# Optimization experiments

Hardware: AMD Instinct MI355X
Metric: run time of the kernel (lower is better)

Reference implementation:

```python
import jax, jax.numpy as jnp
import numpy as np

N = 50000      # cells (nodes)
E = 800000     # kNN edges
IN = 50        # PCA dims
HID = 64       # hidden_dim
HEADS = 4
C = HID // HEADS  # per-head channels = 16
L = 3          # num_layers
NC = 12        # num_classes
INV_SQRT_C = 1.0 / np.sqrt(C)
LN_EPS = 1e-5


def setup_inputs() -> dict:
    key = jax.random.key(0)
    ks = iter(jax.random.split(key, 32))
    def w(shape, fan_in):
        return jax.random.normal(next(ks), shape, jnp.float32) / np.sqrt(fan_in)
    inp = {
        'x': jax.random.normal(next(ks), (N, IN), jnp.float32),
        'edge_index': jax.random.randint(next(ks), (2, E), 0, N, jnp.int32),
        'edge_attr': jax.random.uniform(next(ks), (E,), jnp.float32),
        # input projection
        'Win': w((IN, HID), IN), 'b_in': jnp.zeros((HID,), jnp.float32),
        # per-layer TransformerConv params (stacked over L)
        'Wq': w((L, HID, HID), HID), 'bq': jnp.zeros((L, HID), jnp.float32),
        'Wk': w((L, HID, HID), HID), 'bk': jnp.zeros((L, HID), jnp.float32),
        'Wv': w((L, HID, HID), HID), 'bv': jnp.zeros((L, HID), jnp.float32),
        'Wedge': w((L, 1, HID), 1),                      # lin_edge, bias=False
        'Wskip': w((L, HID, HID), HID), 'bskip': jnp.zeros((L, HID), jnp.float32),
        'Wbeta': w((L, 3 * HID, 1), 3 * HID),            # lin_beta, bias=False
        'ln_g': jnp.ones((L, HID), jnp.float32), 'ln_b': jnp.zeros((L, HID), jnp.float32),
        # classifier MLP
        'Wc1': w((HID, HID), HID), 'bc1': jnp.zeros((HID,), jnp.float32),
        'Wc2': w((HID, NC), HID), 'bc2': jnp.zeros((NC,), jnp.float32),
    }
    return inp


def _layer_norm(z, g, b):
    mu = z.mean(-1, keepdims=True)
    var = ((z - mu) ** 2).mean(-1, keepdims=True)
    return (z - mu) / jnp.sqrt(var + LN_EPS) * g + b


def reference(x, edge_index, edge_attr, Win, b_in, Wq, bq, Wk, bk, Wv, bv,
              Wedge, Wskip, bskip, Wbeta, ln_g, ln_b, Wc1, bc1, Wc2, bc2):
    n = x.shape[0]
    src, dst = edge_index[0], edge_index[1]   # messages flow src -> dst
    ea = edge_attr[:, None]                    # (E,1)
    h = x @ Win + b_in                         # (N,HID)
    for i in range(L):
        h_res = h
        q = (h @ Wq[i] + bq[i]).reshape(n, HEADS, C)
        k = (h @ Wk[i] + bk[i]).reshape(n, HEADS, C)
        v = (h @ Wv[i] + bv[i]).reshape(n, HEADS, C)
        e = (ea @ Wedge[i]).reshape(-1, HEADS, C)        # (E,H,C)
        kj = k[src] + e                                   # edge-gathered keys + edge feat
        alpha = jnp.einsum('ehc,ehc->eh', q[dst], kj) * INV_SQRT_C  # (E,H)
        # segment softmax over destination nodes
        amax = jax.ops.segment_max(alpha, dst, num_segments=n)
        amax = jnp.where(jnp.isfinite(amax), amax, 0.0)
        ex = jnp.exp(alpha - amax[dst])
        denom = jax.ops.segment_sum(ex, dst, num_segments=n)
        p = ex / (denom[dst] + 1e-16)
        msg = (v[src] + e) * p[..., None]                 # (E,H,C)
        out = jax.ops.segment_sum(msg, dst, num_segments=n).reshape(n, HID)
        # beta-gated skip
        x_r = h @ Wskip[i] + bskip[i]
        beta = jax.nn.sigmoid(jnp.concatenate([out, x_r, out - x_r], -1) @ Wbeta[i])  # (N,1)
        out = beta * x_r + (1.0 - beta) * out
        h = _layer_norm(out + h_res, ln_g[i], ln_b[i])
    h1 = jax.nn.relu(h @ Wc1 + bc1)
    return h1 @ Wc2 + bc2
```

## Files before the change

### kernel.cpp

```cpp
#include <hip/hip_runtime.h>
#include <hip/hip_fp16.h>
#include <math.h>

#define IN_F 50
#define HID 64
#define NC 12
#define LN_EPS 1e-5f

#define BSH 8
#define BSZ 256
#define CHUNK 8192
#define PCAP 8192

typedef _Float16 half8 __attribute__((ext_vector_type(8)));
typedef _Float16 half4_t __attribute__((ext_vector_type(4)));
typedef float float4v __attribute__((ext_vector_type(4)));


__global__ void count_kernel(const int* __restrict__ dst, int* __restrict__ cnt, int e) {
  int i = blockIdx.x * blockDim.x + threadIdx.x;
  if (i < e) atomicAdd(&cnt[dst[i]], 1);
}

__global__ __launch_bounds__(256) void scan_reduce_kernel(const int* __restrict__ cnt,
                                                          int* __restrict__ part, int n) {
  int base = blockIdx.x * 1024;
  int sum = 0;
  for (int i = threadIdx.x; i < 1024; i += 256) {
    int g = base + i;
    if (g < n) sum += cnt[g];
  }
#pragma unroll
  for (int off = 1; off < 64; off <<= 1) sum += __shfl_xor(sum, off);
  __shared__ int ws[4];
  if ((threadIdx.x & 63) == 0) ws[threadIdx.x >> 6] = sum;
  __syncthreads();
  if (threadIdx.x == 0) part[blockIdx.x] = ws[0] + ws[1] + ws[2] + ws[3];
}

__global__ void scan_part_kernel(int* __restrict__ part, int nb, int* __restrict__ total) {
  int lane = threadIdx.x;
  int orig = (lane < nb) ? part[lane] : 0;
  int v = orig;
#pragma unroll
  for (int off = 1; off < 64; off <<= 1) {
    int t = __shfl_up(v, off);
    if (lane >= off) v += t;
  }
  if (lane < nb) part[lane] = v - orig;
  if (lane == 63) *total = v;
}

__global__ __launch_bounds__(256) void scan_apply_kernel(const int* __restrict__ cnt,
    const int* __restrict__ part, int* __restrict__ rowptr, int n) {
  int base = blockIdx.x * 1024;
  int t = threadIdx.x;
  int vals[4];
  int lsum = 0;
#pragma unroll
  for (int j = 0; j < 4; j++) {
    int g = base + t * 4 + j;
    vals[j] = (g < n) ? cnt[g] : 0;
    lsum += vals[j];
  }
  int v = lsum;
#pragma unroll
  for (int off = 1; off < 64; off <<= 1) {
    int tv = __shfl_up(v, off);
    if ((t & 63) >= off) v += tv;
  }
  __shared__ int wsum[4];
  if ((t & 63) == 63) wsum[t >> 6] = v;
  __syncthreads();
  int wbase = 0;
  int w = t >> 6;
#pragma unroll
  for (int j = 0; j < 4; j++) if (j < w) wbase += wsum[j];
  int excl = v - lsum + wbase + part[blockIdx.x];
#pragma unroll
  for (int j = 0; j < 4; j++) {
    int g = base + t * 4 + j;
    if (g < n) rowptr[g] = excl;
    excl += vals[j];
  }
}

__global__ void cursor_init_kernel(const int* __restrict__ rowptr,
                                   int* __restrict__ cursor, int n, int nbk) {
  int b = blockIdx.x * blockDim.x + threadIdx.x;
  if (b < nbk) cursor[b] = rowptr[min(b * BSZ, n)];
}

__global__ __launch_bounds__(256) void bucket_kernel(
    const int* __restrict__ src, const int* __restrict__ dst,
    const float* __restrict__ ea, int* __restrict__ cursor,
    unsigned long long* __restrict__ rec_stage,
    unsigned short* __restrict__ dloc_stage, int e)
{
  __shared__ int bcnt[256];
  __shared__ int gbase[256];
  __shared__ int bfill[256];
  int tid = threadIdx.x;
  bcnt[tid] = 0; bfill[tid] = 0;
  __syncthreads();
  int cb = blockIdx.x * CHUNK;
  int ce = min(cb + CHUNK, e);
  for (int i = cb + tid; i < ce; i += 256)
    atomicAdd(&bcnt[dst[i] >> BSH], 1);
  __syncthreads();
  if (bcnt[tid] > 0) gbase[tid] = atomicAdd(&cursor[tid], bcnt[tid]);
  __syncthreads();
  for (int i = cb + tid; i < ce; i += 256) {
    int d = dst[i];
    int b = d >> BSH;
    int slot = atomicAdd(&bfill[b], 1);
    int pos = gbase[b] + slot;
    rec_stage[pos] =
        ((unsigned long long)__float_as_uint(ea[i]) << 32) | (unsigned int)src[i];
    dloc_stage[pos] = (unsigned short)(d & (BSZ - 1));
  }
}

__global__ __launch_bounds__(256) void place_kernel(
    const int* __restrict__ rowptr,
    const unsigned long long* __restrict__ rec_stage,
    const unsigned short* __restrict__ dloc_stage,
    unsigned long long* __restrict__ edges, int n)
{
  extern __shared__ char smem[];
  unsigned long long* sbuf = (unsigned long long*)smem;
  int* lrp  = (int*)(smem + (size_t)PCAP * 8);
  int* lcnt = lrp + BSZ;
  int lo = blockIdx.x * BSZ;
  int hi = min(lo + BSZ, n);
  int nb = hi - lo;
  int tid = threadIdx.x;
  if (tid < nb) { lrp[tid] = rowptr[lo + tid]; lcnt[tid] = 0; }
  __syncthreads();
  int base = rowptr[lo];
  int cnt  = rowptr[hi] - base;
  for (int i = tid; i < cnt; i += 256) {
    unsigned long long rec = rec_stage[base + i];
    int dl = dloc_stage[base + i];
    int slot = (lrp[dl] - base) + atomicAdd(&lcnt[dl], 1);
    if (slot < PCAP) sbuf[slot] = rec;
    else edges[(size_t)base + slot] = rec;
  }
  __syncthreads();
  int lim = min(cnt, PCAP);
  for (int i = tid; i < lim; i += 256)
    edges[(size_t)base + i] = sbuf[i];
}


__global__ __launch_bounds__(256) void wprep_kernel(
    const float* __restrict__ Wq, const float* __restrict__ Wk,
    const float* __restrict__ Wv, const float* __restrict__ Ws,
    const float* __restrict__ Wc1, const float* __restrict__ Win,
    const float* __restrict__ bq, const float* __restrict__ bk,
    const float* __restrict__ bv, const float* __restrict__ bs,
    const float* __restrict__ bc1, const float* __restrict__ bin,
    _Float16* __restrict__ Wt, float* __restrict__ biasP)
{
  int idx = blockIdx.x * 256 + threadIdx.x;
  if (idx >= 896 * 64) return;
  int col = idx >> 6, k = idx & 63;
  float w, b;
  if (col < 768) {
    int l = col >> 8, rem = col & 255;
    int mat = rem >> 6, c = rem & 63;
    const float* W  = (mat == 0) ? Wq : (mat == 1) ? Wk : (mat == 2) ? Wv : Ws;
    const float* bb = (mat == 0) ? bq : (mat == 1) ? bk : (mat == 2) ? bv : bs;
    w = W[((size_t)l * 64 + k) * 64 + c];
    b = bb[l * 64 + c];
  } else if (col < 832) {
    int c = col - 768;
    w = Wc1[k * 64 + c];
    b = bc1[c];
  } else {
    int c = col - 832;
    w = (k < IN_F) ? Win[k * 64 + c] : 0.f;
    b = bin[c];
  }
  Wt[idx] = (_Float16)w;
  if (k == 0) biasP[col] = b;
}


template<int NMAT, int MODE, bool RELU>
__global__ __launch_bounds__(256) void gemm_mfma(
    const float* __restrict__ A, int lda, int kin, int M,
    const _Float16* __restrict__ Wt, const float* __restrict__ biasP,
    float* __restrict__ C, int ldc,
    float* __restrict__ qx, __half* __restrict__ kvb)
{
  __shared__ __align__(16) _Float16 hsh[64 * 72];
  constexpr int KVSZ = (MODE == 1) ? 64 * 128 : 8;
  __shared__ __align__(16) __half kvsh[KVSZ];

  const int tid = threadIdx.x;
  const int wave = tid >> 6, lane = tid & 63;
  const int lrow = lane & 15, quad = lane >> 4;
  const int row0 = blockIdx.x * 64;
  constexpr int WPC = 4 / NMAT;
  const int cg = wave / WPC;
  const int wi = wave % WPC;

  half8 bf[4][2];
  const _Float16* wbase = Wt + (size_t)cg * 64 * 64;
#pragma unroll
  for (int ct = 0; ct < 4; ct++)
#pragma unroll
    for (int ks = 0; ks < 2; ks++)
      bf[ct][ks] = *(const half8*)&wbase[(ct * 16 + lrow) * 64 + ks * 32 + quad * 8];
  float bv_[4];
#pragma unroll
  for (int ct = 0; ct < 4; ct++) bv_[ct] = biasP[cg * 64 + ct * 16 + lrow];

  if (kin == 64) {
    int r = tid >> 2, cq = tid & 3;
    int grow = row0 + r;
#pragma unroll
    for (int i = 0; i < 4; i++) {
      int c0 = cq * 16 + i * 4;
      float4 v = make_float4(0.f, 0.f, 0.f, 0.f);
      if (grow < M) v = *(const float4*)&A[(size_t)grow * lda + c0];
      half4_t hv;
      hv[0] = (_Float16)v.x; hv[1] = (_Float16)v.y;
      hv[2] = (_Float16)v.z; hv[3] = (_Float16)v.w;
      *(half4_t*)&hsh[r * 72 + c0] = hv;
    }
  } else {
    for (int idx = tid; idx < 64 * 64; idx += 256) {
      int r = idx >> 6, c = idx & 63;
      int grow = row0 + r;
      float v = (grow < M && c < kin) ? A[(size_t)grow * lda + c] : 0.f;
      hsh[r * 72 + c] = (_Float16)v;
    }
  }
  __syncthreads();

  float4v acc[NMAT][4];
#pragma unroll
  for (int rt = 0; rt < NMAT; rt++)
#pragma unroll
    for (int ct = 0; ct < 4; ct++) {
      acc[rt][ct][0] = bv_[ct]; acc[rt][ct][1] = bv_[ct];
      acc[rt][ct][2] = bv_[ct]; acc[rt][ct][3] = bv_[ct];
    }

#pragma unroll
  for (int rt = 0; rt < NMAT; rt++) {
    int rbase = (wi * NMAT + rt) * 16;
#pragma unroll
    for (int ks = 0; ks < 2; ks++) {
      half8 af = *(const half8*)&hsh[(rbase + lrow) * 72 + ks * 32 + quad * 8];
#pragma unroll
      for (int ct = 0; ct < 4; ct++)
        acc[rt][ct] = __builtin_amdgcn_mfma_f32_16x16x32_f16(af, bf[ct][ks],
                                                             acc[rt][ct], 0, 0, 0);
    }
  }

  if (MODE == 0) {
#pragma unroll
    for (int rt = 0; rt < NMAT; rt++) {
      int rbase = (wi * NMAT + rt) * 16;
#pragma unroll
      for (int reg = 0; reg < 4; reg++) {
        int row = row0 + rbase + quad * 4 + reg;
        if (row < M) {
#pragma unroll
          for (int ct = 0; ct < 4; ct++) {
            float v = acc[rt][ct][reg];
            if (RELU) v = fmaxf(v, 0.f);
            C[(size_t)row * ldc + cg * 64 + ct * 16 + lrow] = v;
          }
        }
      }
    }
  } else {
    if (cg == 0 || cg == 3) {
      int cofs = (cg == 0) ? 0 : 64;
#pragma unroll
      for (int rt = 0; rt < 4; rt++) {
#pragma unroll
        for (int reg = 0; reg < 4; reg++) {
          int row = row0 + rt * 16 + quad * 4 + reg;
          if (row < M) {
#pragma unroll
            for (int ct = 0; ct < 4; ct++)
              qx[(size_t)row * 128 + cofs + ct * 16 + lrow] = acc[rt][ct][reg];
          }
        }
      }
    } else {
      int cofs = (cg == 1) ? 0 : 64;
#pragma unroll
      for (int rt = 0; rt < 4; rt++)
#pragma unroll
        for (int reg = 0; reg < 4; reg++) {
          int rloc = rt * 16 + quad * 4 + reg;
#pragma unroll
          for (int ct = 0; ct < 4; ct++)
            kvsh[rloc * 128 + cofs + ct * 16 + lrow] = __float2half(acc[rt][ct][reg]);
        }
    }
    __syncthreads();
    for (int idx = tid; idx < 1024; idx += 256) {
      int r = idx >> 4, c4 = idx & 15;
      int grow = row0 + r;
      if (grow < M) {
        uint2 kk = *(const uint2*)&kvsh[r * 128 + c4 * 4];
        uint2 vv = *(const uint2*)&kvsh[r * 128 + 64 + c4 * 4];
        uint4 o; o.x = kk.x; o.y = kk.y; o.z = vv.x; o.w = vv.y;
        *(uint4*)&kvb[(size_t)grow * 128 + c4 * 8] = o;
      }
    }
  }
}


__global__ __launch_bounds__(256) void attn_post_kernel(
    const int* __restrict__ rowptr, const unsigned long long* __restrict__ edges,
    const float* __restrict__ qx, const uint4* __restrict__ kvb,
    const float* __restrict__ wedge, const float* __restrict__ wbeta,
    const float* __restrict__ lng, const float* __restrict__ lnb,
    float* __restrict__ h, int n)
{
  int lane = threadIdx.x & 63;
  int node = blockIdx.x * 4 + (threadIdx.x >> 6);
  if (node >= n) return;
  int grp = lane >> 4;
  int c4 = lane & 15;
  const float4* row4 = (const float4*)qx;
  float4 q4 = row4[(size_t)node * 32 + c4];
  float4 we4 = ((const float4*)wedge)[c4];
  const float SC = 0.25f * 1.44269504f;
  float4 qs;
  qs.x = q4.x * SC; qs.y = q4.y * SC; qs.z = q4.z * SC; qs.w = q4.w * SC;
  float qwe = qs.x * we4.x + qs.y * we4.y + qs.z * we4.z + qs.w * we4.w;
  int s0 = rowptr[node], s1 = rowptr[node + 1];
  float l = 0.f, pa = 0.f;
  float ax = 0.f, ay = 0.f, az = 0.f, aw = 0.f;
  for (int cb = s0; cb < s1; cb += 64) {
    int cnt = min(64, s1 - cb);
    unsigned long long rec64 = (lane < cnt) ? edges[cb + lane] : 0ull;
    unsigned int my_src = (unsigned int)(rec64 & 0xffffffffu);
    unsigned int my_ea  = (unsigned int)(rec64 >> 32);
    for (int j = 0; j * 4 < cnt; j++) {
      int sl = j * 4 + grp;
      bool valid = sl < cnt;
      int srcn   = (int)__shfl(my_src, sl);
      float a    = __uint_as_float(__shfl(my_ea, sl));
      uint4 kv = kvb[(size_t)srcn * 16 + c4];
      float2 k01 = __half22float2(*(__half2*)&kv.x);
      float2 k23 = __half22float2(*(__half2*)&kv.y);
      float2 v01 = __half22float2(*(__half2*)&kv.z);
      float2 v23 = __half22float2(*(__half2*)&kv.w);
      float prod = qs.x * k01.x + qs.y * k01.y + qs.z * k23.x + qs.w * k23.y
                 + a * qwe;
      prod += __shfl_xor(prod, 1);
      prod += __shfl_xor(prod, 2);
      float p = valid ? exp2f(prod) : 0.f;
      l  += p;
      pa += p * a;
      ax += p * v01.x;
      ay += p * v01.y;
      az += p * v23.x;
      aw += p * v23.y;
    }
  }
  ax += pa * we4.x; ay += pa * we4.y; az += pa * we4.z; aw += pa * we4.w;
  ax += __shfl_xor(ax, 16); ax += __shfl_xor(ax, 32);
  ay += __shfl_xor(ay, 16); ay += __shfl_xor(ay, 32);
  az += __shfl_xor(az, 16); az += __shfl_xor(az, 32);
  aw += __shfl_xor(aw, 16); aw += __shfl_xor(aw, 32);
  l  += __shfl_xor(l, 16);  l  += __shfl_xor(l, 32);
  float inv = 1.f / (l + 1e-16f);
  float ox = ax * inv, oy = ay * inv, oz = az * inv, ow = aw * inv;
  float4 xr = row4[(size_t)node * 32 + 16 + c4];
  float4 hr = ((const float4*)h)[(size_t)node * 16 + c4];
  float4 w1 = ((const float4*)wbeta)[c4];
  float4 w2 = ((const float4*)wbeta)[16 + c4];
  float4 w3 = ((const float4*)wbeta)[32 + c4];
  float sv = ox * w1.x + oy * w1.y + oz * w1.z + ow * w1.w
           + xr.x * w2.x + xr.y * w2.y + xr.z * w2.z + xr.w * w2.w
           + (ox - xr.x) * w3.x + (oy - xr.y) * w3.y
           + (oz - xr.z) * w3.z + (ow - xr.w) * w3.w;
  sv += __shfl_xor(sv, 1); sv += __shfl_xor(sv, 2);
  sv += __shfl_xor(sv, 4); sv += __shfl_xor(sv, 8);
  float beta = 1.f / (1.f + __expf(-sv));
  float zx = beta * xr.x + (1.f - beta) * ox + hr.x;
  float zy = beta * xr.y + (1.f - beta) * oy + hr.y;
  float zz = beta * xr.z + (1.f - beta) * oz + hr.z;
  float zw = beta * xr.w + (1.f - beta) * ow + hr.w;
  float mu = zx + zy + zz + zw;
  mu += __shfl_xor(mu, 1); mu += __shfl_xor(mu, 2);
  mu += __shfl_xor(mu, 4); mu += __shfl_xor(mu, 8);
  mu *= (1.f / 64.f);
  float dx = zx - mu, dy = zy - mu, dz = zz - mu, dw = zw - mu;
  float var = dx * dx + dy * dy + dz * dz + dw * dw;
  var += __shfl_xor(var, 1); var += __shfl_xor(var, 2);
  var += __shfl_xor(var, 4); var += __shfl_xor(var, 8);
  var *= (1.f / 64.f);
  float rstd = rsqrtf(var + LN_EPS);
  float4 g4 = ((const float4*)lng)[c4];
  float4 b4 = ((const float4*)lnb)[c4];
  if (grp == 0) {
    float4 res;
    res.x = dx * rstd * g4.x + b4.x;
    res.y = dy * rstd * g4.y + b4.y;
    res.z = dz * rstd * g4.z + b4.z;
    res.w = dw * rstd * g4.w + b4.w;
    ((float4*)h)[(size_t)node * 16 + c4] = res;
  }
}


__global__ __launch_bounds__(256) void cls2_kernel(const float* __restrict__ h1,
    const float* __restrict__ Wc2, const float* __restrict__ bc2,
    float* __restrict__ out, int n) {
  __shared__ float W2[HID * NC];
  __shared__ float b2[NC];
  int tid = threadIdx.x;
  for (int i = tid; i < HID * NC; i += 256) W2[i] = Wc2[i];
  if (tid < NC) b2[tid] = bc2[tid];
  __syncthreads();
  int row = blockIdx.x * 256 + tid;
  if (row >= n) return;
  float a[NC];
#pragma unroll
  for (int mm = 0; mm < NC; mm++) a[mm] = b2[mm];
  const float4* hp = (const float4*)(h1 + (size_t)row * HID);
#pragma unroll
  for (int k4 = 0; k4 < 16; k4++) {
    float4 hv = hp[k4];
    float h_[4] = {hv.x, hv.y, hv.z, hv.w};
#pragma unroll
    for (int kk = 0; kk < 4; kk++)
#pragma unroll
      for (int mm = 0; mm < NC; mm++)
        a[mm] = fmaf(h_[kk], W2[(k4 * 4 + kk) * NC + mm], a[mm]);
  }
#pragma unroll
  for (int mm = 0; mm < NC; mm++) out[(size_t)row * NC + mm] = a[mm];
}


extern "C" void kernel_launch(void* const* d_in, const int* in_sizes, int n_in,
                              void* d_out, int out_size, void* d_ws, size_t ws_size,
                              hipStream_t stream) {
  const float* x     = (const float*)d_in[0];
  const int*   eidx  = (const int*)d_in[1];
  const float* eattr = (const float*)d_in[2];
  const float* Win   = (const float*)d_in[3];
  const float* b_in  = (const float*)d_in[4];
  const float* Wq    = (const float*)d_in[5];
  const float* bq    = (const float*)d_in[6];
  const float* Wk    = (const float*)d_in[7];
  const float* bk    = (const float*)d_in[8];
  const float* Wv    = (const float*)d_in[9];
  const float* bv    = (const float*)d_in[10];
  const float* Wedge = (const float*)d_in[11];
  const float* Wskip = (const float*)d_in[12];
  const float* bskip = (const float*)d_in[13];
  const float* Wbeta = (const float*)d_in[14];
  const float* ln_g  = (const float*)d_in[15];
  const float* ln_b  = (const float*)d_in[16];
  const float* Wc1   = (const float*)d_in[17];
  const float* bc1   = (const float*)d_in[18];
  const float* Wc2   = (const float*)d_in[19];
  const float* bc2   = (const float*)d_in[20];
  float* out = (float*)d_out;

  int n = in_sizes[0] / IN_F;
  int e = in_sizes[2];
  const int* src = eidx;
  const int* dstp = eidx + e;

  char* ws = (char*)d_ws;
  size_t off = 0;
  auto alloc = [&](size_t bytes) { void* p = ws + off; off += (bytes + 255) & ~(size_t)255; return p; };
  int*    rowptr = (int*)alloc((size_t)(n + 1) * 4);
  int*    fill   = (int*)alloc((size_t)n * 4);
  int*    part   = (int*)alloc(64 * 4);
  int*    cursor = (int*)alloc(256 * 4);
  unsigned long long* rec_stage = (unsigned long long*)alloc((size_t)e * 8);
  unsigned short*     dloc_stage = (unsigned short*)alloc((size_t)e * 2);
  unsigned long long* edges = (unsigned long long*)alloc((size_t)e * 8);
  float*  h      = (float*)alloc((size_t)n * HID * 4);
  float*  qx     = (float*)alloc((size_t)n * 128 * 4);
  __half* kvb    = (__half*)alloc((size_t)n * 128 * 2);
  float*  h1     = (float*)alloc((size_t)n * HID * 4);
  _Float16* Wt   = (_Float16*)alloc((size_t)896 * 64 * 2);
  float*  biasP  = (float*)alloc(896 * 4);

  int nb  = (n + 1023) / 1024;
  int nbk = (n + BSZ - 1) / BSZ;
  int mtiles = (n + 63) / 64;

  wprep_kernel<<<(896 * 64 + 255) / 256, 256, 0, stream>>>(
      Wq, Wk, Wv, Wskip, Wc1, Win, bq, bk, bv, bskip, bc1, b_in, Wt, biasP);

  (void)hipMemsetAsync(fill, 0, (size_t)n * 4, stream);
  count_kernel<<<(e + 255) / 256, 256, 0, stream>>>(dstp, fill, e);
  scan_reduce_kernel<<<nb, 256, 0, stream>>>(fill, part, n);
  scan_part_kernel<<<1, 64, 0, stream>>>(part, nb, rowptr + n);
  scan_apply_kernel<<<nb, 256, 0, stream>>>(fill, part, rowptr, n);
  cursor_init_kernel<<<1, 256, 0, stream>>>(rowptr, cursor, n, nbk);
  bucket_kernel<<<(e + CHUNK - 1) / CHUNK, 256, 0, stream>>>(
      src, dstp, eattr, cursor, rec_stage, dloc_stage, e);
  size_t psmem = (size_t)PCAP * 8 + BSZ * 8;
  place_kernel<<<nbk, 256, psmem, stream>>>(rowptr, rec_stage, dloc_stage, edges, n);

  gemm_mfma<1, 0, false><<<mtiles, 256, 0, stream>>>(
      x, IN_F, IN_F, n, Wt + (size_t)832 * 64, biasP + 832, h, HID, nullptr, nullptr);

  for (int i = 0; i < 3; i++) {
    gemm_mfma<4, 1, false><<<mtiles, 256, 0, stream>>>(
        h, HID, HID, n, Wt + (size_t)i * 256 * 64, biasP + i * 256,
        nullptr, 0, qx, kvb);
    attn_post_kernel<<<(n + 3) / 4, 256, 0, stream>>>(
        rowptr, edges, qx, (const uint4*)kvb, Wedge + i * HID, Wbeta + i * 3 * HID,
        ln_g + i * HID, ln_b + i * HID, h, n);
  }

  gemm_mfma<1, 0, true><<<mtiles, 256, 0, stream>>>(
      h, HID, HID, n, Wt + (size_t)768 * 64, biasP + 768, h1, HID, nullptr, nullptr);
  cls2_kernel<<<(n + 255) / 256, 256, 0, stream>>>(h1, Wc2, bc2, out, n);
}
```

Baseline: 380.0 us.

## Single-pass bucketed CSR build and fp16 query/skip storage with fdot2 attention

Replaces the count/scan/cursor chain with a bucket pass into fixed-capacity per-bucket slots, a tiny bucket scan, and a place kernel that builds per-node histograms and rowptr in shared memory. The GEMM now writes q (pre-scaled by the softmax constant) and the skip projection in fp16 via shared memory, halving that traffic. The attention loop uses packed fp16 dot instructions and is unrolled. This removes several kernel launches and an atomic pass over all edges, but it assumes no bucket exceeds PCAP edges and lowers the precision of q and x_r.

```diff
diff --git a/kernel.cpp b/kernel.cpp
--- a/kernel.cpp
+++ b/kernel.cpp
@@ -9,87 +9,29 @@
 
 #define BSH 8
 #define BSZ 256
+#define NBK_MAX 256
 #define CHUNK 8192
 #define PCAP 8192
 
+#define SCQ 0.36067376022224085f
+
 typedef _Float16 half8 __attribute__((ext_vector_type(8)));
 typedef _Float16 half4_t __attribute__((ext_vector_type(4)));
+typedef _Float16 half2_t __attribute__((ext_vector_type(2)));
 typedef float float4v __attribute__((ext_vector_type(4)));
 
-
-__global__ void count_kernel(const int* __restrict__ dst, int* __restrict__ cnt, int e) {
-  int i = blockIdx.x * blockDim.x + threadIdx.x;
-  if (i < e) atomicAdd(&cnt[dst[i]], 1);
-}
-
-__global__ __launch_bounds__(256) void scan_reduce_kernel(const int* __restrict__ cnt,
-                                                          int* __restrict__ part, int n) {
-  int base = blockIdx.x * 1024;
-  int sum = 0;
-  for (int i = threadIdx.x; i < 1024; i += 256) {
-    int g = base + i;
-    if (g < n) sum += cnt[g];
-  }
-#pragma unroll
-  for (int off = 1; off < 64; off <<= 1) sum += __shfl_xor(sum, off);
-  __shared__ int ws[4];
-  if ((threadIdx.x & 63) == 0) ws[threadIdx.x >> 6] = sum;
-  __syncthreads();
-  if (threadIdx.x == 0) part[blockIdx.x] = ws[0] + ws[1] + ws[2] + ws[3];
-}
-
-__global__ void scan_part_kernel(int* __restrict__ part, int nb, int* __restrict__ total) {
-  int lane = threadIdx.x;
-  int orig = (lane < nb) ? part[lane] : 0;
-  int v = orig;
-#pragma unroll
-  for (int off = 1; off < 64; off <<= 1) {
-    int t = __shfl_up(v, off);
-    if (lane >= off) v += t;
-  }
-  if (lane < nb) part[lane] = v - orig;
-  if (lane == 63) *total = v;
-}
-
-__global__ __launch_bounds__(256) void scan_apply_kernel(const int* __restrict__ cnt,
-    const int* __restrict__ part, int* __restrict__ rowptr, int n) {
-  int base = blockIdx.x * 1024;
-  int t = threadIdx.x;
-  int vals[4];
-  int lsum = 0;
-#pragma unroll
-  for (int j = 0; j < 4; j++) {
-    int g = base + t * 4 + j;
-    vals[j] = (g < n) ? cnt[g] : 0;
-    lsum += vals[j];
-  }
-  int v = lsum;
-#pragma unroll
-  for (int off = 1; off < 64; off <<= 1) {
-    int tv = __shfl_up(v, off);
-    if ((t & 63) >= off) v += tv;
-  }
-  __shared__ int wsum[4];
-  if ((t & 63) == 63) wsum[t >> 6] = v;
-  __syncthreads();
-  int wbase = 0;
-  int w = t >> 6;
-#pragma unroll
-  for (int j = 0; j < 4; j++) if (j < w) wbase += wsum[j];
-  int excl = v - lsum + wbase + part[blockIdx.x];
-#pragma unroll
-  for (int j = 0; j < 4; j++) {
-    int g = base + t * 4 + j;
-    if (g < n) rowptr[g] = excl;
-    excl += vals[j];
-  }
-}
-
-__global__ void cursor_init_kernel(const int* __restrict__ rowptr,
-                                   int* __restrict__ cursor, int n, int nbk) {
-  int b = blockIdx.x * blockDim.x + threadIdx.x;
-  if (b < nbk) cursor[b] = rowptr[min(b * BSZ, n)];
-}
+static __device__ __forceinline__ half2_t h2cast(unsigned int u) {
+  return __builtin_bit_cast(half2_t, u);
+}
+
+#if __has_builtin(__builtin_amdgcn_fdot2)
+#define FDOT2(a, b, c) __builtin_amdgcn_fdot2((a), (b), (c), false)
+#else
+static __device__ __forceinline__ float FDOT2(half2_t a, half2_t b, float c) {
+  return (float)a[0] * (float)b[0] + (float)a[1] * (float)b[1] + c;
+}
+#endif
+
 
 __global__ __launch_bounds__(256) void bucket_kernel(
     const int* __restrict__ src, const int* __restrict__ dst,
@@ -114,41 +56,85 @@
     int d = dst[i];
     int b = d >> BSH;
     int slot = atomicAdd(&bfill[b], 1);
-    int pos = gbase[b] + slot;
+    size_t pos = (size_t)b * PCAP + gbase[b] + slot;
     rec_stage[pos] =
         ((unsigned long long)__float_as_uint(ea[i]) << 32) | (unsigned int)src[i];
     dloc_stage[pos] = (unsigned short)(d & (BSZ - 1));
   }
 }
 
+__global__ __launch_bounds__(256) void scanb_kernel(
+    const int* __restrict__ cursor, int* __restrict__ bbase,
+    int* __restrict__ rowptr_n, int nbk)
+{
+  int t = threadIdx.x;
+  int v = (t < nbk) ? cursor[t] : 0;
+  int incl = v;
+#pragma unroll
+  for (int off = 1; off < 64; off <<= 1) {
+    int tv = __shfl_up(incl, off);
+    if ((t & 63) >= off) incl += tv;
+  }
+  __shared__ int ws[4];
+  if ((t & 63) == 63) ws[t >> 6] = incl;
+  __syncthreads();
+  int wb = 0;
+  int w = t >> 6;
+#pragma unroll
+  for (int j = 0; j < 4; j++) if (j < w) wb += ws[j];
+  int excl = incl - v + wb;
+  if (t < nbk) bbase[t] = excl;
+  if (t == 255) *rowptr_n = excl;
+}
+
 __global__ __launch_bounds__(256) void place_kernel(
-    const int* __restrict__ rowptr,
+    const int* __restrict__ cursor, const int* __restrict__ bbase,
     const unsigned long long* __restrict__ rec_stage,
     const unsigned short* __restrict__ dloc_stage,
-    unsigned long long* __restrict__ edges, int n)
+    unsigned long long* __restrict__ edges, int* __restrict__ rowptr, int n)
 {
   extern __shared__ char smem[];
   unsigned long long* sbuf = (unsigned long long*)smem;
-  int* lrp  = (int*)(smem + (size_t)PCAP * 8);
-  int* lcnt = lrp + BSZ;
-  int lo = blockIdx.x * BSZ;
+  int* hist = (int*)(smem + (size_t)PCAP * 8);
+  int* lcnt = hist + 256;
+  __shared__ int ws[4];
+  int b = blockIdx.x;
+  int t = threadIdx.x;
+  int lo = b * BSZ;
   int hi = min(lo + BSZ, n);
-  int nb = hi - lo;
-  int tid = threadIdx.x;
-  if (tid < nb) { lrp[tid] = rowptr[lo + tid]; lcnt[tid] = 0; }
-  __syncthreads();
-  int base = rowptr[lo];
-  int cnt  = rowptr[hi] - base;
-  for (int i = tid; i < cnt; i += 256) {
-    unsigned long long rec = rec_stage[base + i];
-    int dl = dloc_stage[base + i];
-    int slot = (lrp[dl] - base) + atomicAdd(&lcnt[dl], 1);
-    if (slot < PCAP) sbuf[slot] = rec;
-    else edges[(size_t)base + slot] = rec;
-  }
-  __syncthreads();
-  int lim = min(cnt, PCAP);
-  for (int i = tid; i < lim; i += 256)
+  int cnt  = cursor[b];
+  int base = bbase[b];
+  size_t bofs = (size_t)b * PCAP;
+  hist[t] = 0;
+  __syncthreads();
+  for (int i = t; i < cnt; i += 256)
+    atomicAdd(&hist[dloc_stage[bofs + i]], 1);
+  __syncthreads();
+  int v = hist[t];
+  int incl = v;
+#pragma unroll
+  for (int off = 1; off < 64; off <<= 1) {
+    int tv = __shfl_up(incl, off);
+    if ((t & 63) >= off) incl += tv;
+  }
+  if ((t & 63) == 63) ws[t >> 6] = incl;
+  __syncthreads();
+  int wb = 0;
+  int w = t >> 6;
+#pragma unroll
+  for (int j = 0; j < 4; j++) if (j < w) wb += ws[j];
+  int excl = incl - v + wb;
+  if (lo + t < hi) rowptr[lo + t] = base + excl;
+  lcnt[t] = excl;
+  __syncthreads();
+  for (int i = t; i < cnt; i += 256) {
+    unsigned long long rec = rec_stage[bofs + i];
+    int dl = dloc_stage[bofs + i];
+    int slot = atomicAdd(&lcnt[dl], 1);
+    sbuf[slot] = rec;
+  }
+  __syncthreads();
+  for (int i = t; i < cnt; i += 256)
     edges[(size_t)base + i] = sbuf[i];
 }
 
@@ -192,11 +178,12 @@
     const float* __restrict__ A, int lda, int kin, int M,
     const _Float16* __restrict__ Wt, const float* __restrict__ biasP,
     float* __restrict__ C, int ldc,
-    float* __restrict__ qx, __half* __restrict__ kvb)
+    __half* __restrict__ qxh, __half* __restrict__ kvb)
 {
   __shared__ __align__(16) _Float16 hsh[64 * 72];
   constexpr int KVSZ = (MODE == 1) ? 64 * 128 : 8;
   __shared__ __align__(16) __half kvsh[KVSZ];
+  __shared__ __align__(16) __half qxsh[KVSZ];
 
   const int tid = threadIdx.x;
   const int wave = tid >> 6, lane = tid & 63;
@@ -280,32 +267,19 @@
       }
     }
   } else {
-    if (cg == 0 || cg == 3) {
-      int cofs = (cg == 0) ? 0 : 64;
-#pragma unroll
-      for (int rt = 0; rt < 4; rt++) {
-#pragma unroll
-        for (int reg = 0; reg < 4; reg++) {
-          int row = row0 + rt * 16 + quad * 4 + reg;
-          if (row < M) {
-#pragma unroll
-            for (int ct = 0; ct < 4; ct++)
-              qx[(size_t)row * 128 + cofs + ct * 16 + lrow] = acc[rt][ct][reg];
-          }
-        }
+    __half* dstsh = (cg == 0 || cg == 3) ? qxsh : kvsh;
+    int cofs = (cg == 0 || cg == 1) ? 0 : 64;
+    float scale = (cg == 0) ? SCQ : 1.f;
+#pragma unroll
+    for (int rt = 0; rt < 4; rt++)
+#pragma unroll
+      for (int reg = 0; reg < 4; reg++) {
+        int rloc = rt * 16 + quad * 4 + reg;
+#pragma unroll
+        for (int ct = 0; ct < 4; ct++)
+          dstsh[rloc * 128 + cofs + ct * 16 + lrow] =
+              __float2half(acc[rt][ct][reg] * scale);
       }
-    } else {
-      int cofs = (cg == 1) ? 0 : 64;
-#pragma unroll
-      for (int rt = 0; rt < 4; rt++)
-#pragma unroll
-        for (int reg = 0; reg < 4; reg++) {
-          int rloc = rt * 16 + quad * 4 + reg;
-#pragma unroll
-          for (int ct = 0; ct < 4; ct++)
-            kvsh[rloc * 128 + cofs + ct * 16 + lrow] = __float2half(acc[rt][ct][reg]);
-        }
-    }
     __syncthreads();
     for (int idx = tid; idx < 1024; idx += 256) {
       int r = idx >> 4, c4 = idx & 15;
@@ -317,13 +291,20 @@
         *(uint4*)&kvb[(size_t)grow * 128 + c4 * 8] = o;
       }
     }
+    for (int idx = tid; idx < 1024; idx += 256) {
+      int r = idx >> 4, g8 = idx & 15;
+      int grow = row0 + r;
+      if (grow < M)
+        *(uint4*)&qxh[(size_t)grow * 128 + g8 * 8] =
+            *(const uint4*)&qxsh[r * 128 + g8 * 8];
+    }
   }
 }
 
 
 __global__ __launch_bounds__(256) void attn_post_kernel(
     const int* __restrict__ rowptr, const unsigned long long* __restrict__ edges,
-    const float* __restrict__ qx, const uint4* __restrict__ kvb,
+    const __half* __restrict__ qxh, const uint4* __restrict__ kvb,
     const float* __restrict__ wedge, const float* __restrict__ wbeta,
     const float* __restrict__ lng, const float* __restrict__ lnb,
     float* __restrict__ h, int n)
@@ -333,13 +314,13 @@
   if (node >= n) return;
   int grp = lane >> 4;
   int c4 = lane & 15;
-  const float4* row4 = (const float4*)qx;
-  float4 q4 = row4[(size_t)node * 32 + c4];
+  const __half* qrow = qxh + (size_t)node * 128;
+  uint2 qu = ((const uint2*)qrow)[c4];
+  half2_t qh01 = h2cast(qu.x), qh23 = h2cast(qu.y);
+  float qf0 = (float)qh01[0], qf1 = (float)qh01[1];
+  float qf2 = (float)qh23[0], qf3 = (float)qh23[1];
   float4 we4 = ((const float4*)wedge)[c4];
-  const float SC = 0.25f * 1.44269504f;
-  float4 qs;
-  qs.x = q4.x * SC; qs.y = q4.y * SC; qs.z = q4.z * SC; qs.w = q4.w * SC;
-  float qwe = qs.x * we4.x + qs.y * we4.y + qs.z * we4.z + qs.w * we4.w;
+  float qwe = qf0 * we4.x + qf1 * we4.y + qf2 * we4.z + qf3 * we4.w;
   int s0 = rowptr[node], s1 = rowptr[node + 1];
   float l = 0.f, pa = 0.f;
   float ax = 0.f, ay = 0.f, az = 0.f, aw = 0.f;
@@ -348,27 +329,26 @@
     unsigned long long rec64 = (lane < cnt) ? edges[cb + lane] : 0ull;
     unsigned int my_src = (unsigned int)(rec64 & 0xffffffffu);
     unsigned int my_ea  = (unsigned int)(rec64 >> 32);
+#pragma unroll 2
     for (int j = 0; j * 4 < cnt; j++) {
       int sl = j * 4 + grp;
       bool valid = sl < cnt;
       int srcn   = (int)__shfl(my_src, sl);
       float a    = __uint_as_float(__shfl(my_ea, sl));
       uint4 kv = kvb[(size_t)srcn * 16 + c4];
-      float2 k01 = __half22float2(*(__half2*)&kv.x);
-      float2 k23 = __half22float2(*(__half2*)&kv.y);
-      float2 v01 = __half22float2(*(__half2*)&kv.z);
-      float2 v23 = __half22float2(*(__half2*)&kv.w);
-      float prod = qs.x * k01.x + qs.y * k01.y + qs.z * k23.x + qs.w * k23.y
-                 + a * qwe;
+      float prod = a * qwe;
+      prod = FDOT2(qh01, h2cast(kv.x), prod);
+      prod = FDOT2(qh23, h2cast(kv.y), prod);
       prod += __shfl_xor(prod, 1);
       prod += __shfl_xor(prod, 2);
       float p = valid ? exp2f(prod) : 0.f;
+      half2_t v01 = h2cast(kv.z), v23 = h2cast(kv.w);
       l  += p;
-      pa += p * a;
-      ax += p * v01.x;
-      ay += p * v01.y;
-      az += p * v23.x;
-      aw += p * v23.y;
+      pa = fmaf(p, a, pa);
+      ax = fmaf(p, (float)v01[0], ax);
+      ay = fmaf(p, (float)v01[1], ay);
+      az = fmaf(p, (float)v23[0], az);
+      aw = fmaf(p, (float)v23[1], aw);
     }
   }
   ax += pa * we4.x; ay += pa * we4.y; az += pa * we4.z; aw += pa * we4.w;
@@ -379,7 +359,11 @@
   l  += __shfl_xor(l, 16);  l  += __shfl_xor(l, 32);
   float inv = 1.f / (l + 1e-16f);
   float ox = ax * inv, oy = ay * inv, oz = az * inv, ow = aw * inv;
-  float4 xr = row4[(size_t)node * 32 + 16 + c4];
+  uint2 xu = ((const uint2*)(qrow + 64))[c4];
+  half2_t x01 = h2cast(xu.x), x23 = h2cast(xu.y);
+  float4 xr;
+  xr.x = (float)x01[0]; xr.y = (float)x01[1];
+  xr.z = (float)x23[0]; xr.w = (float)x23[1];
   float4 hr = ((const float4*)h)[(size_t)node * 16 + c4];
   float4 w1 = ((const float4*)wbeta)[c4];
   float4 w2 = ((const float4*)wbeta)[16 + c4];
@@ -482,37 +466,33 @@
   char* ws = (char*)d_ws;
   size_t off = 0;
   auto alloc = [&](size_t bytes) { void* p = ws + off; off += (bytes + 255) & ~(size_t)255; return p; };
+  int nbk = (n + BSZ - 1) / BSZ;
+
   int*    rowptr = (int*)alloc((size_t)(n + 1) * 4);
-  int*    fill   = (int*)alloc((size_t)n * 4);
-  int*    part   = (int*)alloc(64 * 4);
-  int*    cursor = (int*)alloc(256 * 4);
-  unsigned long long* rec_stage = (unsigned long long*)alloc((size_t)e * 8);
-  unsigned short*     dloc_stage = (unsigned short*)alloc((size_t)e * 2);
+  int*    cursor = (int*)alloc(NBK_MAX * 4);
+  int*    bbase  = (int*)alloc(NBK_MAX * 4);
+  unsigned long long* rec_stage = (unsigned long long*)alloc((size_t)nbk * PCAP * 8);
+  unsigned short*     dloc_stage = (unsigned short*)alloc((size_t)nbk * PCAP * 2);
   unsigned long long* edges = (unsigned long long*)alloc((size_t)e * 8);
   float*  h      = (float*)alloc((size_t)n * HID * 4);
-  float*  qx     = (float*)alloc((size_t)n * 128 * 4);
+  __half* qxh    = (__half*)alloc((size_t)n * 128 * 2);
   __half* kvb    = (__half*)alloc((size_t)n * 128 * 2);
   float*  h1     = (float*)alloc((size_t)n * HID * 4);
   _Float16* Wt   = (_Float16*)alloc((size_t)896 * 64 * 2);
   float*  biasP  = (float*)alloc(896 * 4);
 
-  int nb  = (n + 1023) / 1024;
-  int nbk = (n + BSZ - 1) / BSZ;
   int mtiles = (n + 63) / 64;
 
   wprep_kernel<<<(896 * 64 + 255) / 256, 256, 0, stream>>>(
       Wq, Wk, Wv, Wskip, Wc1, Win, bq, bk, bv, bskip, bc1, b_in, Wt, biasP);
 
-  (void)hipMemsetAsync(fill, 0, (size_t)n * 4, stream);
-  count_kernel<<<(e + 255) / 256, 256, 0, stream>>>(dstp, fill, e);
-  scan_reduce_kernel<<<nb, 256, 0, stream>>>(fill, part, n);
-  scan_part_kernel<<<1, 64, 0, stream>>>(part, nb, rowptr + n);
-  scan_apply_kernel<<<nb, 256, 0, stream>>>(fill, part, rowptr, n);
-  cursor_init_kernel<<<1, 256, 0, stream>>>(rowptr, cursor, n, nbk);
+  (void)hipMemsetAsync(cursor, 0, NBK_MAX * 4, stream);
   bucket_kernel<<<(e + CHUNK - 1) / CHUNK, 256, 0, stream>>>(
       src, dstp, eattr, cursor, rec_stage, dloc_stage, e);
-  size_t psmem = (size_t)PCAP * 8 + BSZ * 8;
-  place_kernel<<<nbk, 256, psmem, stream>>>(rowptr, rec_stage, dloc_stage, edges, n);
+  scanb_kernel<<<1, 256, 0, stream>>>(cursor, bbase, rowptr + n, nbk);
+  size_t psmem = (size_t)PCAP * 8 + 512 * 4;
+  place_kernel<<<nbk, 256, psmem, stream>>>(
+      cursor, bbase, rec_stage, dloc_stage, edges, rowptr, n);
 
   gemm_mfma<1, 0, false><<<mtiles, 256, 0, stream>>>(
       x, IN_F, IN_F, n, Wt + (size_t)832 * 64, biasP + 832, h, HID, nullptr, nullptr);
@@ -520,9 +500,9 @@
   for (int i = 0; i < 3; i++) {
     gemm_mfma<4, 1, false><<<mtiles, 256, 0, stream>>>(
         h, HID, HID, n, Wt + (size_t)i * 256 * 64, biasP + i * 256,
-        nullptr, 0, qx, kvb);
+        nullptr, 0, qxh, kvb);
     attn_post_kernel<<<(n + 3) / 4, 256, 0, stream>>>(
-        rowptr, edges, qx, (const uint4*)kvb, Wedge + i * HID, Wbeta + i * 3 * HID,
+        rowptr, edges, qxh, (const uint4*)kvb, Wedge + i * HID, Wbeta + i * 3 * HID,
         ln_g + i * HID, ln_b + i * HID, h, n);
   }
 
```

Measured after the change: 340.0 us. -10.5%, faster.
